# Kernel optimization log

Hardware: AMD Instinct MI355X
Metric: run time of the kernel (lower is better)

The kernel has to match this reference:

```python
import jax, jax.numpy as jnp
import numpy as np


def _dense_image_warp(img, flow):
    """Faithful port of tfa.image.dense_image_warp (bilinear interpolate_bilinear).
    img:  [B,H,W,C] float
    flow: [B,H,W,2] float, output[b,h,w] = img sampled at (h - flow[...,0], w - flow[...,1])
    """
    B, H, W, C = img.shape
    grid_y = jnp.arange(H, dtype=img.dtype)[None, :, None]   # [1,H,1]
    grid_x = jnp.arange(W, dtype=img.dtype)[None, None, :]   # [1,1,W]
    qy = grid_y - flow[..., 0]  # [B,H,W] query rows
    qx = grid_x - flow[..., 1]  # [B,H,W] query cols

    # tfa interpolate_bilinear: floor clipped to [0, size-2], alpha clipped to [0,1]
    fy = jnp.clip(jnp.floor(qy), 0.0, H - 2)
    fx = jnp.clip(jnp.floor(qx), 0.0, W - 2)
    ay = jnp.clip(qy - fy, 0.0, 1.0)[..., None]  # [B,H,W,1]
    ax = jnp.clip(qx - fx, 0.0, 1.0)[..., None]
    iy = fy.astype(jnp.int32)
    ix = fx.astype(jnp.int32)

    b = jnp.arange(B, dtype=jnp.int32)[:, None, None]  # [B,1,1] broadcast over H,W
    top_left     = img[b, iy,     ix]      # [B,H,W,C]
    top_right    = img[b, iy,     ix + 1]
    bottom_left  = img[b, iy + 1, ix]
    bottom_right = img[b, iy + 1, ix + 1]

    interp_top    = top_left + ax * (top_right - top_left)
    interp_bottom = bottom_left + ax * (bottom_right - bottom_left)
    return interp_top + ay * (interp_bottom - interp_top)


def setup_inputs() -> dict:
    key = jax.random.key(0)
    k1, k2 = jax.random.split(key)
    B, H, W, C = 8, 512, 512, 16
    x = jax.random.normal(k1, (B, H, W, C), dtype=jnp.float32)
    # scale flow so displacements span a realistic few-pixel range
    flow = jax.random.normal(k2, (B, H, W, 2), dtype=jnp.float32) * 5.0
    return {"x": x, "flow": flow}


def reference(x, flow):
    return _dense_image_warp(x, flow)
```

## Files before the change

kernel.cpp:

```cpp
#include <hip/hip_runtime.h>


constexpr int B = 8;
constexpr int H = 512;
constexpr int W = 512;
constexpr int C = 16;

__global__ __launch_bounds__(256) void warp_kernel(
    const float* __restrict__ img,
    const float* __restrict__ flow,
    float* __restrict__ out)
{
    const int tid = blockIdx.x * blockDim.x + threadIdx.x;
    const int p  = tid >> 2;
    const int c0 = (tid & 3) << 2;

    const int w = p & (W - 1);
    const int h = (p >> 9) & (H - 1);
    const int b = p >> 18;

    const float2 f = *reinterpret_cast<const float2*>(flow + 2 * (size_t)p);

    const float qy = (float)h - f.x;
    const float qx = (float)w - f.y;

    float fy = fminf(fmaxf(floorf(qy), 0.0f), (float)(H - 2));
    float fx = fminf(fmaxf(floorf(qx), 0.0f), (float)(W - 2));
    const float ay = fminf(fmaxf(qy - fy, 0.0f), 1.0f);
    const float ax = fminf(fmaxf(qx - fx, 0.0f), 1.0f);
    const int iy = (int)fy;
    const int ix = (int)fx;

    const size_t rowStride = (size_t)W * C;
    const float* base = img + ((size_t)((b * H + iy) * W + ix) * C + c0);

    const float4 tl = *reinterpret_cast<const float4*>(base);
    const float4 tr = *reinterpret_cast<const float4*>(base + C);
    const float4 bl = *reinterpret_cast<const float4*>(base + rowStride);
    const float4 br = *reinterpret_cast<const float4*>(base + rowStride + C);

    float4 o;
    {
        const float t0 = tl.x + ax * (tr.x - tl.x);
        const float b0 = bl.x + ax * (br.x - bl.x);
        o.x = t0 + ay * (b0 - t0);
    }
    {
        const float t1 = tl.y + ax * (tr.y - tl.y);
        const float b1 = bl.y + ax * (br.y - bl.y);
        o.y = t1 + ay * (b1 - t1);
    }
    {
        const float t2 = tl.z + ax * (tr.z - tl.z);
        const float b2 = bl.z + ax * (br.z - bl.z);
        o.z = t2 + ay * (b2 - t2);
    }
    {
        const float t3 = tl.w + ax * (tr.w - tl.w);
        const float b3 = bl.w + ax * (br.w - bl.w);
        o.w = t3 + ay * (b3 - t3);
    }

    *reinterpret_cast<float4*>(out + (size_t)p * C + c0) = o;
}

extern "C" void kernel_launch(void* const* d_in, const int* in_sizes, int n_in,
                              void* d_out, int out_size, void* d_ws, size_t ws_size,
                              hipStream_t stream) {
    const float* img  = (const float*)d_in[0];
    const float* flow = (const float*)d_in[1];
    float* out = (float*)d_out;

    const int total = B * H * W * 4;
    const int block = 256;
    const int grid = total / block;
    warp_kernel<<<grid, block, 0, stream>>>(img, flow, out);
}
```

Baseline: 252.5 us.

## Map blocks to 8x8 spatial tiles interleaved across batch, use nontemporal flow/out accesses

Each block now covers an 8x8 pixel tile instead of two image rows. Consecutive block IDs cycle through the batch index first, so neighbouring blocks work on different images. The 2D tile is meant to improve cache locality of the gathered neighbour pixels, since flows of a few pixels point into a compact region rather than a long row strip. Flow loads and output stores use nontemporal hints so these streaming accesses do not pollute the cache, and the math is vectorised with ext_vector types. Interleaving batches across consecutive blocks may spread the working set and reduce L2 reuse between adjacent tiles.

```diff
diff --git a/kernel.cpp b/kernel.cpp
--- a/kernel.cpp
+++ b/kernel.cpp
@@ -5,27 +5,37 @@
 constexpr int H = 512;
 constexpr int W = 512;
 constexpr int C = 16;
+constexpr int TILE = 8;
 
-__global__ __launch_bounds__(256) void warp_kernel(
+typedef float vf2 __attribute__((ext_vector_type(2)));
+typedef float vf4 __attribute__((ext_vector_type(4)));
+
+__global__ __launch_bounds__(256, 8) void warp_kernel(
     const float* __restrict__ img,
     const float* __restrict__ flow,
     float* __restrict__ out)
 {
-    const int tid = blockIdx.x * blockDim.x + threadIdx.x;
-    const int p  = tid >> 2;
-    const int c0 = (tid & 3) << 2;
+    const int bid = blockIdx.x;
+    const int b  = bid & 7;
+    const int t  = bid >> 3;
+    const int h0 = (t >> 6) << 3;
+    const int w0 = (t & 63) << 3;
 
-    const int w = p & (W - 1);
-    const int h = (p >> 9) & (H - 1);
-    const int b = p >> 18;
+    const int quad = threadIdx.x >> 2;
+    const int c0   = (threadIdx.x & 3) << 2;
 
-    const float2 f = *reinterpret_cast<const float2*>(flow + 2 * (size_t)p);
+    const int h = h0 + (quad >> 3);
+    const int w = w0 + (quad & 7);
+    const size_t p = ((size_t)(b * H + h)) * W + w;
+
+    const vf2 f = __builtin_nontemporal_load(
+        reinterpret_cast<const vf2*>(flow + 2 * p));
 
     const float qy = (float)h - f.x;
     const float qx = (float)w - f.y;
 
-    float fy = fminf(fmaxf(floorf(qy), 0.0f), (float)(H - 2));
-    float fx = fminf(fmaxf(floorf(qx), 0.0f), (float)(W - 2));
+    const float fy = fminf(fmaxf(floorf(qy), 0.0f), (float)(H - 2));
+    const float fx = fminf(fmaxf(floorf(qx), 0.0f), (float)(W - 2));
     const float ay = fminf(fmaxf(qy - fy, 0.0f), 1.0f);
     const float ax = fminf(fmaxf(qx - fx, 0.0f), 1.0f);
     const int iy = (int)fy;
@@ -34,34 +44,17 @@
     const size_t rowStride = (size_t)W * C;
     const float* base = img + ((size_t)((b * H + iy) * W + ix) * C + c0);
 
-    const float4 tl = *reinterpret_cast<const float4*>(base);
-    const float4 tr = *reinterpret_cast<const float4*>(base + C);
-    const float4 bl = *reinterpret_cast<const float4*>(base + rowStride);
-    const float4 br = *reinterpret_cast<const float4*>(base + rowStride + C);
+    const vf4 tl = *reinterpret_cast<const vf4*>(base);
+    const vf4 tr = *reinterpret_cast<const vf4*>(base + C);
+    const vf4 bl = *reinterpret_cast<const vf4*>(base + rowStride);
+    const vf4 br = *reinterpret_cast<const vf4*>(base + rowStride + C);
 
-    float4 o;
-    {
-        const float t0 = tl.x + ax * (tr.x - tl.x);
-        const float b0 = bl.x + ax * (br.x - bl.x);
-        o.x = t0 + ay * (b0 - t0);
-    }
-    {
-        const float t1 = tl.y + ax * (tr.y - tl.y);
-        const float b1 = bl.y + ax * (br.y - bl.y);
-        o.y = t1 + ay * (b1 - t1);
-    }
-    {
-        const float t2 = tl.z + ax * (tr.z - tl.z);
-        const float b2 = bl.z + ax * (br.z - bl.z);
-        o.z = t2 + ay * (b2 - t2);
-    }
-    {
-        const float t3 = tl.w + ax * (tr.w - tl.w);
-        const float b3 = bl.w + ax * (br.w - bl.w);
-        o.w = t3 + ay * (b3 - t3);
-    }
+    const vf4 tv = tl + ax * (tr - tl);
+    const vf4 bv = bl + ax * (br - bl);
+    const vf4 o  = tv + ay * (bv - tv);
 
-    *reinterpret_cast<float4*>(out + (size_t)p * C + c0) = o;
+    __builtin_nontemporal_store(
+        o, reinterpret_cast<vf4*>(out + p * C + c0));
 }
 
 extern "C" void kernel_launch(void* const* d_in, const int* in_sizes, int n_in,
@@ -71,8 +64,6 @@
     const float* flow = (const float*)d_in[1];
     float* out = (float*)d_out;
 
-    const int total = B * H * W * 4;
-    const int block = 256;
-    const int grid = total / block;
-    warp_kernel<<<grid, block, 0, stream>>>(img, flow, out);
+    const int grid = B * (H / TILE) * (W / TILE);
+    warp_kernel<<<grid, 256, 0, stream>>>(img, flow, out);
 }
```

After: 260.0 us. +3.0%, slower.
